# Kernel tuning notes

Hardware: AMD Instinct MI355X
Metric: run time of the kernel (lower is better)

Reference implementation:

```python
import jax, jax.numpy as jnp
import numpy as np

IN_DIM = 256
QK_DIM = 64

def setup_inputs() -> dict:
    key = jax.random.key(0)
    ks = jax.random.split(key, 7)
    b, c, h, w = 16, IN_DIM, 96, 96
    x = jax.random.normal(ks[0], (b, c, h, w), dtype=jnp.float32)
    sc = 1.0 / np.sqrt(c)
    Wq = jax.random.normal(ks[1], (QK_DIM, c), dtype=jnp.float32) * sc
    bq = jax.random.normal(ks[2], (QK_DIM,), dtype=jnp.float32) * 0.01
    Wk = jax.random.normal(ks[3], (QK_DIM, c), dtype=jnp.float32) * sc
    bk = jax.random.normal(ks[4], (QK_DIM,), dtype=jnp.float32) * 0.01
    Wv = jax.random.normal(ks[5], (c, c), dtype=jnp.float32) * sc
    bv = jax.random.normal(ks[6], (c,), dtype=jnp.float32) * 0.01
    gamma = jnp.zeros((1,), dtype=jnp.float32) + 0.5  # nonzero so output depends on attention
    return {"x": x, "Wq": Wq, "bq": bq, "Wk": Wk, "bk": bk, "Wv": Wv, "bv": bv, "gamma": gamma}

def reference(x, Wq, bq, Wk, bk, Wv, bv, gamma):
    # 1x1-conv projections: (b,c,h,w) -> (b,q,h,w)
    Q = jnp.einsum('bchw,qc->bqhw', x, Wq) + bq[None, :, None, None]
    K = jnp.einsum('bchw,qc->bqhw', x, Wk) + bk[None, :, None, None]
    V = jnp.einsum('bchw,vc->bvhw', x, Wv) + bv[None, :, None, None]
    # column attention over height h, per (batch, width) column; unscaled scores
    scores = jnp.einsum('bqhw,bqgw->bwhg', Q, K)        # (b, w, h, h)
    attn = jax.nn.softmax(scores, axis=-1)
    # out[:, :, i] = sum_j V[:, :, j] * attn[i, j]  (bmm with attn transposed)
    out = jnp.einsum('bcgw,bwhg->bchw', V, attn)
    return gamma[0] * out + x
```

## Files before the change

### kernel.cpp

```cpp
#include <hip/hip_runtime.h>
#include <stdint.h>

#define DI __device__ __forceinline__

typedef __attribute__((ext_vector_type(4))) float f4;
typedef __attribute__((ext_vector_type(4))) float f32x4;
typedef _Float16 f16;
typedef __attribute__((ext_vector_type(8))) f16 f16x8;

static constexpr int BATCH = 16, C = 256, H = 96, W = 96, QK = 64, F = 384;
static constexpr int P = H * W;

static constexpr size_t OFF_WC = 0;
static constexpr size_t OFF_BC = OFF_WC + (size_t)F * C * 2;
static constexpr size_t OFF_QP = OFF_BC + 4096;
static constexpr size_t OFF_KP = OFF_QP + (size_t)BATCH * P * QK * 2;
static constexpr size_t OFF_VP = OFF_KP + (size_t)BATCH * P * QK * 2;
static constexpr size_t OFF_O1 = OFF_VP + (size_t)BATCH * P * C * 2;
static constexpr size_t WS_END = OFF_O1 + (size_t)BATCH * P * C * 2;

DI void gll16(const void* g, void* l) {
  __builtin_amdgcn_global_load_lds((const __attribute__((address_space(1))) void*)g,
                                   (__attribute__((address_space(3))) void*)l, 16, 0, 0);
}
DI f32x4 mfma16(f16x8 a, f16x8 b, f32x4 c) {
  return __builtin_amdgcn_mfma_f32_16x16x32_f16(a, b, c, 0, 0, 0);
}
DI int mod13(int v) {
  return v - 13 * ((v * 5042) >> 16);
}

__global__ __launch_bounds__(256) void wprep_kernel(
    const float* __restrict__ Wq, const float* __restrict__ bq,
    const float* __restrict__ Wk, const float* __restrict__ bk,
    const float* __restrict__ Wv, const float* __restrict__ bv,
    f16* __restrict__ Wc, float* __restrict__ bc) {
  const int f = blockIdx.x, t = threadIdx.x;
  const float* src; int row;
  if (f < 64)       { src = Wq; row = f; }
  else if (f < 128) { src = Wk; row = f - 64; }
  else              { src = Wv; row = f - 128; }
  Wc[f * C + t] = (f16)src[row * C + t];
  if (t == 0) bc[f] = (f < 64) ? bq[f] : (f < 128) ? bk[f - 64] : bv[f - 128];
}

__global__ __launch_bounds__(256, 2) void gemm_qkv(
    const float* __restrict__ x, const f16* __restrict__ Wc, const float* __restrict__ bc,
    f16* __restrict__ Qp, f16* __restrict__ Kp, f16* __restrict__ Vp) {
  __shared__ f16 As[2][128 * 72];
  __shared__ f16 Bs[2][128 * 64];
  const int tid = threadIdx.x, lane = tid & 63, wv = tid >> 6;
  const int wm = wv >> 1, wn = wv & 1;
  const int c2 = ((blockIdx.x & 7) * 432) + (blockIdx.x >> 3);
  const int b = c2 / 216, r = c2 % 216;
  const int mt = r / 3, nt = r % 3;
  const int m0 = mt * 128, f0 = nt * 128;
  const float* Ax = x + (size_t)b * C * P + m0;
  const f16* Bb = Wc + (size_t)f0 * C;

  const int ap = tid & 127;
  const int ach = tid >> 7;
  const int grow = lane >> 3, lblk = (lane & 7) ^ grow;

  f32x4 acc[4][4];
#pragma unroll
  for (int i = 0; i < 4; ++i)
#pragma unroll
    for (int j = 0; j < 4; ++j) acc[i][j] = (f32x4){0.f, 0.f, 0.f, 0.f};

  float av[4][8];
  auto loadA = [&](int k0) {
#pragma unroll
    for (int s = 0; s < 4; ++s) {
      const int c = k0 + (s * 2 + ach) * 8;
#pragma unroll
      for (int u = 0; u < 8; ++u) av[s][u] = Ax[(size_t)(c + u) * P + ap];
    }
  };
  auto writeA = [&](int bsel) {
#pragma unroll
    for (int s = 0; s < 4; ++s) {
      const int cb = s * 2 + ach;
      f16x8 hv;
#pragma unroll
      for (int u = 0; u < 8; ++u) hv[u] = (f16)av[s][u];
      *reinterpret_cast<f16x8*>(&As[bsel][ap * 72 + cb * 8]) = hv;
    }
  };
  auto stageB = [&](int k0, int bsel) {
#pragma unroll
    for (int s = 0; s < 4; ++s) {
      const int rbase = wv * 32 + s * 8;
      gll16(Bb + (size_t)(rbase + grow) * C + k0 + lblk * 8, &Bs[bsel][rbase * 64]);
    }
  };
  auto compute = [&](int bsel) {
#pragma unroll
    for (int ks = 0; ks < 2; ++ks) {
      const int kb = ks * 4 + (lane >> 4);
      f16x8 a[4], bb[4];
#pragma unroll
      for (int i = 0; i < 4; ++i) {
        const int row = wm * 64 + i * 16 + (lane & 15);
        a[i] = *reinterpret_cast<const f16x8*>(&As[bsel][row * 72 + kb * 8]);
      }
#pragma unroll
      for (int j = 0; j < 4; ++j) {
        const int row = wn * 64 + j * 16 + (lane & 15);
        bb[j] = *reinterpret_cast<const f16x8*>(&Bs[bsel][row * 64 + ((kb ^ (row & 7)) << 3)]);
      }
#pragma unroll
      for (int i = 0; i < 4; ++i)
#pragma unroll
        for (int j = 0; j < 4; ++j) acc[i][j] = mfma16(a[i], bb[j], acc[i][j]);
    }
  };

  loadA(0);
  stageB(0, 0);
  writeA(0);
  __syncthreads();
  int buf = 0;
#pragma unroll
  for (int t = 0; t < 3; ++t) {
    loadA((t + 1) * 64);
    stageB((t + 1) * 64, buf ^ 1);
    compute(buf);
    writeA(buf ^ 1);
    __syncthreads();
    buf ^= 1;
  }
  compute(buf);

#pragma unroll
  for (int j = 0; j < 4; ++j) {
    const int fl = wn * 64 + j * 16 + (lane & 15);
    const float bias = bc[f0 + fl];
#pragma unroll
    for (int i = 0; i < 4; ++i) {
#pragma unroll
      for (int q = 0; q < 4; ++q) {
        const int p = m0 + wm * 64 + i * 16 + ((lane >> 4) << 2) + q;
        const float v = acc[i][j][q] + bias;
        if (nt == 0) {
          if (fl < 64) Qp[((size_t)b * P + p) * QK + fl] = (f16)v;
          else         Kp[((size_t)b * P + p) * QK + (fl - 64)] = (f16)v;
        } else {
          Vp[((size_t)b * P + p) * C + (nt - 1) * 128 + fl] = (f16)v;
        }
      }
    }
  }
}

__global__ __launch_bounds__(256, 2) void attn_kernel(
    const f16* __restrict__ Qp, const f16* __restrict__ Kp, const f16* __restrict__ Vp,
    f16* __restrict__ O1) {
  __shared__ char smem[24576 + 53248 + 768 + 768];
  f16*   qs   = (f16*)smem;
  f16*   ksm  = (f16*)(smem + 12288);
  f16*   sP   = (f16*)smem;
  f16*   vt   = (f16*)(smem + 24576);
  float* redm = (float*)(smem + 24576 + 53248);
  float* reds = redm + 192;

  const int tid = threadIdx.x, lane = tid & 63, wv = tid >> 6;
  const int wmq = wv >> 1, wnq = wv & 1;
  const int id = ((blockIdx.x & 7) * 192) + (blockIdx.x >> 3);
  const int b = id / 96, w = id % 96;

  const int cc = tid;
  f16 vv[96];
#pragma unroll
  for (int g = 0; g < 96; ++g)
    vv[g] = Vp[((size_t)b * P + g * 96 + w) * C + cc];

  {
    const int grow = lane >> 3;
    const int lblk = (lane & 7) ^ grow;
#pragma unroll
    for (int s = 0; s < 3; ++s) {
      const int sec = wv * 3 + s;
      const int row = sec * 8 + grow;
      const size_t src = ((size_t)b * P + (size_t)row * 96 + w) * QK + lblk * 8;
      gll16(Qp + src, &qs[sec * 512]);
      gll16(Kp + src, &ksm[sec * 512]);
    }
  }
  {
    const int r13 = mod13(cc);
#pragma unroll
    for (int ob = 0; ob < 12; ++ob) {
      int phys = ob + r13;
      if (phys >= 13) phys -= 13;
      f16x8 pk;
#pragma unroll
      for (int e = 0; e < 8; ++e) pk[e] = vv[ob * 8 + e];
      *reinterpret_cast<f16x8*>(&vt[cc * 104 + phys * 8]) = pk;
    }
  }
  __syncthreads();

  f32x4 acc[3][3];
#pragma unroll
  for (int i = 0; i < 3; ++i)
#pragma unroll
    for (int j = 0; j < 3; ++j) acc[i][j] = (f32x4){0.f, 0.f, 0.f, 0.f};
#pragma unroll
  for (int ks = 0; ks < 2; ++ks) {
    const int kb = ks * 4 + (lane >> 4);
    f16x8 a[3], bb[3];
#pragma unroll
    for (int i = 0; i < 3; ++i) {
      const int row = wmq * 48 + i * 16 + (lane & 15);
      a[i] = *reinterpret_cast<const f16x8*>(&qs[row * 64 + ((kb ^ (row & 7)) << 3)]);
    }
#pragma unroll
    for (int j = 0; j < 3; ++j) {
      const int row = wnq * 48 + j * 16 + (lane & 15);
      bb[j] = *reinterpret_cast<const f16x8*>(&ksm[row * 64 + ((kb ^ (row & 7)) << 3)]);
    }
#pragma unroll
    for (int i = 0; i < 3; ++i)
#pragma unroll
      for (int j = 0; j < 3; ++j) acc[i][j] = mfma16(a[i], bb[j], acc[i][j]);
  }

#pragma unroll
  for (int i = 0; i < 3; ++i)
#pragma unroll
    for (int q = 0; q < 4; ++q) {
      float m = fmaxf(fmaxf(acc[i][0][q], acc[i][1][q]), acc[i][2][q]);
#pragma unroll
      for (int o = 8; o >= 1; o >>= 1) m = fmaxf(m, __shfl_xor(m, o, 64));
      if ((lane & 15) == 0)
        redm[wnq * 96 + wmq * 48 + i * 16 + ((lane >> 4) << 2) + q] = m;
    }
  __syncthreads();
#pragma unroll
  for (int i = 0; i < 3; ++i)
#pragma unroll
    for (int q = 0; q < 4; ++q) {
      const int h = wmq * 48 + i * 16 + ((lane >> 4) << 2) + q;
      const float m = fmaxf(redm[h], redm[96 + h]);
      float s = 0.f;
#pragma unroll
      for (int j = 0; j < 3; ++j) {
        const float p = __expf(acc[i][j][q] - m);
        acc[i][j][q] = p;
        s += p;
      }
#pragma unroll
      for (int o = 8; o >= 1; o >>= 1) s += __shfl_xor(s, o, 64);
      if ((lane & 15) == 0) reds[wnq * 96 + h] = s;
    }
#pragma unroll
  for (int i = 0; i < 3; ++i)
#pragma unroll
    for (int q = 0; q < 4; ++q) {
      const int h = wmq * 48 + i * 16 + ((lane >> 4) << 2) + q;
#pragma unroll
      for (int j = 0; j < 3; ++j) {
        const int g = wnq * 48 + j * 16 + (lane & 15);
        sP[h * 128 + (((g >> 3) ^ (h & 7)) << 3) + (g & 7)] = (f16)acc[i][j][q];
      }
    }
  __syncthreads();

  {
    f32x4 o[3][8];
#pragma unroll
    for (int i = 0; i < 3; ++i)
#pragma unroll
      for (int j = 0; j < 8; ++j) o[i][j] = (f32x4){0.f, 0.f, 0.f, 0.f};
#pragma unroll
    for (int ks = 0; ks < 3; ++ks) {
      const int gb = ks * 4 + (lane >> 4);
      f16x8 a[3];
#pragma unroll
      for (int i = 0; i < 3; ++i) {
        const int row = wmq * 48 + i * 16 + (lane & 15);
        a[i] = *reinterpret_cast<const f16x8*>(&sP[row * 128 + ((gb ^ (row & 7)) << 3)]);
      }
#pragma unroll
      for (int j = 0; j < 8; ++j) {
        const int crow = wnq * 128 + j * 16 + (lane & 15);
        int phys = gb + mod13(crow);
        if (phys >= 13) phys -= 13;
        const f16x8 bv = *reinterpret_cast<const f16x8*>(&vt[crow * 104 + phys * 8]);
#pragma unroll
        for (int i = 0; i < 3; ++i) o[i][j] = mfma16(a[i], bv, o[i][j]);
      }
    }
    f16* ob_ = O1 + ((size_t)b * 96 + w) * 96 * C;
#pragma unroll
    for (int i = 0; i < 3; ++i) {
#pragma unroll
      for (int q = 0; q < 4; ++q) {
        const int h = wmq * 48 + i * 16 + ((lane >> 4) << 2) + q;
        const float rs = 1.0f / (reds[h] + reds[96 + h]);
#pragma unroll
        for (int j = 0; j < 8; ++j) {
          const int c = wnq * 128 + j * 16 + (lane & 15);
          ob_[(size_t)h * C + c] = (f16)(o[i][j][q] * rs);
        }
      }
    }
  }
}

__global__ __launch_bounds__(256, 3) void epi_kernel(
    const f16* __restrict__ O1, const float* __restrict__ x,
    const float* __restrict__ gamma, float* __restrict__ out) {
  __shared__ f16 t[96 * 256];
  const int id = ((blockIdx.x & 7) * 192) + (blockIdx.x >> 3);
  const int b = id / 96, h = id % 96;
  const int tid = threadIdx.x, lane = tid & 63, wv = tid >> 6;
  {
    const int grow = lane >> 5;
#pragma unroll
    for (int s = 0; s < 12; ++s) {
      const int sec = wv * 12 + s;
      const int row = sec * 2 + grow;
      const int lblk = (lane & 31) ^ (row & 31);
      gll16(O1 + (((size_t)b * 96 + row) * 96 + h) * C + lblk * 8, &t[sec * 512]);
    }
  }
  __syncthreads();
  const float g = gamma[0];
#pragma unroll
  for (int pass = 0; pass < 24; ++pass) {
    const int idx = pass * 256 + tid;
    const int c = idx / 24, wc = idx % 24;
    const int w4 = wc * 4;
    const size_t o = (((size_t)b * C + c) * H + h) * W + w4;
    const f4 xv = *reinterpret_cast<const f4*>(x + o);
    f4 r;
#pragma unroll
    for (int u = 0; u < 4; ++u) {
      const int wr = w4 + u;
      const f16 hv = t[wr * 256 + (((c >> 3) ^ (wr & 31)) << 3) + (c & 7)];
      r[u] = g * (float)hv + xv[u];
    }
    *reinterpret_cast<f4*>(out + o) = r;
  }
}

extern "C" void kernel_launch(void* const* d_in, const int* in_sizes, int n_in,
                              void* d_out, int out_size, void* d_ws, size_t ws_size,
                              hipStream_t stream) {
  const float* x     = (const float*)d_in[0];
  const float* Wq    = (const float*)d_in[1];
  const float* bq    = (const float*)d_in[2];
  const float* Wk    = (const float*)d_in[3];
  const float* bk    = (const float*)d_in[4];
  const float* Wv    = (const float*)d_in[5];
  const float* bv    = (const float*)d_in[6];
  const float* gamma = (const float*)d_in[7];
  float* out = (float*)d_out;
  char* ws = (char*)d_ws;
  if (ws_size < WS_END) return;

  f16*   Wc = (f16*)(ws + OFF_WC);
  float* bc = (float*)(ws + OFF_BC);
  f16*   Qp = (f16*)(ws + OFF_QP);
  f16*   Kp = (f16*)(ws + OFF_KP);
  f16*   Vp = (f16*)(ws + OFF_VP);
  f16*   O1 = (f16*)(ws + OFF_O1);

  wprep_kernel<<<dim3(F), dim3(256), 0, stream>>>(Wq, bq, Wk, bk, Wv, bv, Wc, bc);
  gemm_qkv<<<dim3(3456), dim3(256), 0, stream>>>(x, Wc, bc, Qp, Kp, Vp);
  attn_kernel<<<dim3(BATCH * 96), dim3(256), 0, stream>>>(Qp, Kp, Vp, O1);
  epi_kernel<<<dim3(BATCH * 96), dim3(256), 0, stream>>>(O1, x, gamma, out);
}
```

Baseline: 425.0 us.

## Load QKV GEMM weights directly into registers and shrink LDS for occupancy

The weight tile is no longer staged through shared memory. Each wave now loads its B fragments straight from global memory into registers, so only the A tile stays in LDS. The A tile switches from a padded layout to an XOR-swizzled 64-wide layout, and its global loads become float2 reads covering two pixels per thread. The smaller LDS footprint lets launch bounds ask for three blocks per CU instead of two. In exchange, B loads are no longer prefetched a stage ahead and are repeated by every wave, which adds global/L2 traffic and register pressure.

Result: slower. 459.0 us (+8.0%).

```diff
diff --git a/kernel.cpp b/kernel.cpp
--- a/kernel.cpp
+++ b/kernel.cpp
@@ -4,6 +4,7 @@
 #define DI __device__ __forceinline__
 
 typedef __attribute__((ext_vector_type(4))) float f4;
+typedef __attribute__((ext_vector_type(2))) float f2;
 typedef __attribute__((ext_vector_type(4))) float f32x4;
 typedef _Float16 f16;
 typedef __attribute__((ext_vector_type(8))) f16 f16x8;
@@ -44,11 +45,10 @@
   if (t == 0) bc[f] = (f < 64) ? bq[f] : (f < 128) ? bk[f - 64] : bv[f - 128];
 }
 
-__global__ __launch_bounds__(256, 2) void gemm_qkv(
+__global__ __launch_bounds__(256, 3) void gemm_qkv(
     const float* __restrict__ x, const f16* __restrict__ Wc, const float* __restrict__ bc,
     f16* __restrict__ Qp, f16* __restrict__ Kp, f16* __restrict__ Vp) {
-  __shared__ f16 As[2][128 * 72];
-  __shared__ f16 Bs[2][128 * 64];
+  __shared__ f16 As[2][128 * 64];
   const int tid = threadIdx.x, lane = tid & 63, wv = tid >> 6;
   const int wm = wv >> 1, wn = wv & 1;
   const int c2 = ((blockIdx.x & 7) * 432) + (blockIdx.x >> 3);
@@ -56,11 +56,9 @@
   const int mt = r / 3, nt = r % 3;
   const int m0 = mt * 128, f0 = nt * 128;
   const float* Ax = x + (size_t)b * C * P + m0;
-  const f16* Bb = Wc + (size_t)f0 * C;
-
-  const int ap = tid & 127;
-  const int ach = tid >> 7;
-  const int grow = lane >> 3, lblk = (lane & 7) ^ grow;
+
+  const int pp = (tid & 63) * 2;
+  const int cq = tid >> 6;
 
   f32x4 acc[4][4];
 #pragma unroll
@@ -68,68 +66,70 @@
 #pragma unroll
     for (int j = 0; j < 4; ++j) acc[i][j] = (f32x4){0.f, 0.f, 0.f, 0.f};
 
-  float av[4][8];
+  f2 av[16];
+  f16x8 breg[2][4];
+
   auto loadA = [&](int k0) {
 #pragma unroll
-    for (int s = 0; s < 4; ++s) {
-      const int c = k0 + (s * 2 + ach) * 8;
-#pragma unroll
-      for (int u = 0; u < 8; ++u) av[s][u] = Ax[(size_t)(c + u) * P + ap];
-    }
+    for (int u = 0; u < 16; ++u)
+      av[u] = *reinterpret_cast<const f2*>(Ax + (size_t)(k0 + cq * 16 + u) * P + pp);
   };
   auto writeA = [&](int bsel) {
 #pragma unroll
-    for (int s = 0; s < 4; ++s) {
-      const int cb = s * 2 + ach;
-      f16x8 hv;
-#pragma unroll
-      for (int u = 0; u < 8; ++u) hv[u] = (f16)av[s][u];
-      *reinterpret_cast<f16x8*>(&As[bsel][ap * 72 + cb * 8]) = hv;
+    for (int rr = 0; rr < 2; ++rr) {
+      const int p = pp + rr;
+#pragma unroll
+      for (int ob = 0; ob < 2; ++ob) {
+        const int cb = cq * 2 + ob;
+        f16x8 hv;
+#pragma unroll
+        for (int u = 0; u < 8; ++u) hv[u] = (f16)av[ob * 8 + u][rr];
+        *reinterpret_cast<f16x8*>(&As[bsel][p * 64 + ((cb ^ (p & 7)) << 3)]) = hv;
+      }
     }
   };
-  auto stageB = [&](int k0, int bsel) {
-#pragma unroll
-    for (int s = 0; s < 4; ++s) {
-      const int rbase = wv * 32 + s * 8;
-      gll16(Bb + (size_t)(rbase + grow) * C + k0 + lblk * 8, &Bs[bsel][rbase * 64]);
+  auto loadB = [&](int k0) {
+#pragma unroll
+    for (int ks = 0; ks < 2; ++ks) {
+      const int kb = ks * 4 + (lane >> 4);
+#pragma unroll
+      for (int j = 0; j < 4; ++j) {
+        const int row = f0 + wn * 64 + j * 16 + (lane & 15);
+        breg[ks][j] = *reinterpret_cast<const f16x8*>(&Wc[(size_t)row * C + k0 + kb * 8]);
+      }
     }
   };
   auto compute = [&](int bsel) {
 #pragma unroll
     for (int ks = 0; ks < 2; ++ks) {
       const int kb = ks * 4 + (lane >> 4);
-      f16x8 a[4], bb[4];
+      f16x8 a[4];
 #pragma unroll
       for (int i = 0; i < 4; ++i) {
         const int row = wm * 64 + i * 16 + (lane & 15);
-        a[i] = *reinterpret_cast<const f16x8*>(&As[bsel][row * 72 + kb * 8]);
-      }
-#pragma unroll
-      for (int j = 0; j < 4; ++j) {
-        const int row = wn * 64 + j * 16 + (lane & 15);
-        bb[j] = *reinterpret_cast<const f16x8*>(&Bs[bsel][row * 64 + ((kb ^ (row & 7)) << 3)]);
+        a[i] = *reinterpret_cast<const f16x8*>(&As[bsel][row * 64 + ((kb ^ (row & 7)) << 3)]);
       }
 #pragma unroll
       for (int i = 0; i < 4; ++i)
 #pragma unroll
-        for (int j = 0; j < 4; ++j) acc[i][j] = mfma16(a[i], bb[j], acc[i][j]);
+        for (int j = 0; j < 4; ++j) acc[i][j] = mfma16(a[i], breg[ks][j], acc[i][j]);
     }
   };
 
   loadA(0);
-  stageB(0, 0);
   writeA(0);
   __syncthreads();
   int buf = 0;
 #pragma unroll
   for (int t = 0; t < 3; ++t) {
+    loadB(t * 64);
     loadA((t + 1) * 64);
-    stageB((t + 1) * 64, buf ^ 1);
     compute(buf);
     writeA(buf ^ 1);
     __syncthreads();
     buf ^= 1;
   }
+  loadB(192);
   compute(buf);
 
 #pragma unroll
```
